# Kernel tuning notes

Measured on AMD Instinct MI355X. Metric: run time of the kernel, lower is better.

Reference implementation:

```python
import jax, jax.numpy as jnp
from jax import lax
import numpy as np

NUM_GROUPS = 16
GN_EPS = 1e-5
POOL = 4
CLAMP_MIN, CLAMP_MAX = 0.0, 1.0


def setup_inputs() -> dict:
    key = jax.random.key(0)
    ks = jax.random.split(key, 6)
    B, Cin, H, W = 128, 8, 128, 128
    Cout, K = 64, 3
    return {
        "x": jax.random.normal(ks[0], (B, Cin, H, W), dtype=jnp.float32),
        "conv_weight": jax.random.normal(ks[1], (Cout, Cin, K, K), dtype=jnp.float32) * 0.1,
        "conv_bias": jax.random.normal(ks[2], (Cout,), dtype=jnp.float32) * 0.1,
        "gn_weight": jax.random.normal(ks[3], (Cout,), dtype=jnp.float32) * 0.1 + 1.0,
        "gn_bias": jax.random.normal(ks[4], (Cout,), dtype=jnp.float32) * 0.1,
        "scale": jax.random.normal(ks[5], (Cout, 1, 1), dtype=jnp.float32) * 0.1 + 1.0,
    }


def reference(x, conv_weight, conv_bias, gn_weight, gn_bias, scale):
    # Conv2d, stride=1, padding=0 (VALID)
    y = lax.conv_general_dilated(
        x, conv_weight, window_strides=(1, 1), padding="VALID",
        dimension_numbers=("NCHW", "OIHW", "NCHW"))
    y = y + conv_bias[None, :, None, None]
    B, C, H, W = y.shape  # (128, 64, 126, 126)
    # GroupNorm: stats per (sample, group)
    yg = y.reshape(B, NUM_GROUPS, -1)
    mean = jnp.mean(yg, axis=-1, keepdims=True)
    var = jnp.mean(jnp.square(yg - mean), axis=-1, keepdims=True)
    yn = ((yg - mean) * lax.rsqrt(var + GN_EPS)).reshape(B, C, H, W)
    yn = yn * gn_weight[None, :, None, None] + gn_bias[None, :, None, None]
    # per-channel scale, shape (C,1,1)
    yn = yn * scale[None]
    # MaxPool2d(kernel=4, stride=4, no padding, floor mode)
    p = lax.reduce_window(yn, -jnp.inf, lax.max,
                          window_dimensions=(1, 1, POOL, POOL),
                          window_strides=(1, 1, POOL, POOL),
                          padding="VALID")
    return jnp.clip(p, CLAMP_MIN, CLAMP_MAX)
```

## Files before the change

kernel.cpp:

```cpp
#include <hip/hip_runtime.h>

typedef __attribute__((ext_vector_type(8))) short short8v;
typedef __attribute__((ext_vector_type(4))) float f32x4;
typedef __attribute__((ext_vector_type(4))) int i32x4;

#define BATCH 128
#define CIN 8
#define HW 128
#define COUT 64
#define OHW 126
#define NG 16
#define PH 31
#define GN_EPS 1e-5f

#define ROWS_A 8
#define STRIPS_A 16
#define INROWS_A 11
#define ACOLS 132

static __device__ __forceinline__ unsigned short f2bf(float f) {
    unsigned u = __float_as_uint(f);
    return (unsigned short)((u + 0x7fffu + ((u >> 16) & 1u)) >> 16);
}
static __device__ __forceinline__ unsigned pk2(float a, float b) {
    return (unsigned)f2bf(a) | ((unsigned)f2bf(b) << 16);
}

__global__ __launch_bounds__(256) void prep_weights(
    const float* __restrict__ w, const float* __restrict__ gnw,
    const float* __restrict__ scale, short* __restrict__ Bpack)
{
    for (int e = threadIdx.x; e < 3 * 4 * 64; e += 256) {
        int dx = e >> 8;
        int nt = (e >> 6) & 3;
        int l  = e & 63;
        int i = l & 15, g = l >> 4;
        int n = nt * 16 + i;
        float sg = copysignf(1.f, gnw[n] * scale[n]);
        #pragma unroll
        for (int j = 0; j < 8; ++j) {
            float v = (g < 3) ? w[((n * CIN + j) * 3 + g) * 3 + dx] * sg : 0.f;
            Bpack[e * 8 + j] = (short)f2bf(v);
        }
    }
}

__global__ __launch_bounds__(256, 4) void conv_fused(
    const float* __restrict__ x, const short* __restrict__ Bpack,
    const float* __restrict__ bias, const float* __restrict__ gnw,
    const float* __restrict__ scale, float* __restrict__ part,
    float* __restrict__ mzbuf)
{
    __shared__ __align__(16) short Abuf[INROWS_A][ACOLS][8];
    __shared__ float red[4][NG][2];
    const int strip = blockIdx.x, b = blockIdx.y;
    const int tid = threadIdx.x, wave = tid >> 6, lane = tid & 63;
    const int i = lane & 15, g = lane >> 4;
    const int r0 = strip * ROWS_A;

    short8v bq[3][4];
    {
        const i32x4* bp = (const i32x4*)Bpack;
        #pragma unroll
        for (int dx = 0; dx < 3; ++dx)
            #pragma unroll
            for (int nt = 0; nt < 4; ++nt) {
                i32x4 v = bp[(dx * 4 + nt) * 64 + lane];
                bq[dx][nt] = *(short8v*)&v;
            }
    }
    float sgn[4], bs2[4], bsg[4];
    #pragma unroll
    for (int nt = 0; nt < 4; ++nt) {
        int c = nt * 16 + i;
        float bc = bias[c];
        float sg = copysignf(1.f, gnw[c] * scale[c]);
        sgn[nt] = sg;
        bs2[nt] = 2.f * bc;
        bsg[nt] = sg * bc;
    }

    {
        const float* xb = x + (size_t)b * CIN * HW * HW;
        for (int e = tid; e < INROWS_A * ACOLS; e += 256) {
            int row = e / ACOLS, col = e % ACOLS;
            int ri = r0 + row;
            bool ok = (row < 10) && (ri < HW) && (col < HW);
            unsigned pk0, pk1, pk2_, pk3;
            {
                const float* base = &xb[(size_t)ri * HW + col];
                float v0 = ok ? base[0 * HW * HW] : 0.f;
                float v1 = ok ? base[1 * HW * HW] : 0.f;
                float v2 = ok ? base[2 * HW * HW] : 0.f;
                float v3 = ok ? base[3 * HW * HW] : 0.f;
                float v4 = ok ? base[4 * HW * HW] : 0.f;
                float v5 = ok ? base[5 * HW * HW] : 0.f;
                float v6 = ok ? base[6 * HW * HW] : 0.f;
                float v7 = ok ? base[7 * HW * HW] : 0.f;
                pk0  = pk2(v0, v1);
                pk1  = pk2(v2, v3);
                pk2_ = pk2(v4, v5);
                pk3  = pk2(v6, v7);
            }
            uint4 w4 = make_uint4(pk0, pk1, pk2_, pk3);
            *(uint4*)&Abuf[row][col][0] = w4;
        }
    }
    __syncthreads();

    float s1[4] = {0.f, 0.f, 0.f, 0.f}, s2[4] = {0.f, 0.f, 0.f, 0.f};
    const int myprow = wave & 1;
    const int tbase  = (wave >> 1) * 4;
    const int prow_g = strip * 2 + myprow;

    for (int tl = 0; tl < 4; ++tl) {
        const int t = tbase + tl;
        float mz[4] = {-3e38f, -3e38f, -3e38f, -3e38f};
        #pragma unroll
        for (int ri_ = 0; ri_ < 4; ++ri_) {
            const int rloc = 4 * myprow + ri_;
            if (r0 + rloc < OHW) {
                f32x4 acc[4];
                #pragma unroll
                for (int nt = 0; nt < 4; ++nt) acc[nt] = (f32x4){0.f, 0.f, 0.f, 0.f};
                #pragma unroll
                for (int dx = 0; dx < 3; ++dx) {
                    short8v a = *(const short8v*)&Abuf[rloc + g][16 * t + i + dx][0];
                    #pragma unroll
                    for (int nt = 0; nt < 4; ++nt)
                        acc[nt] = __builtin_amdgcn_mfma_f32_16x16x32_bf16(a, bq[dx][nt], acc[nt], 0, 0, 0);
                }
                const int nv = (t == 7 && g == 3) ? 2 : 4;
                #pragma unroll
                for (int nt = 0; nt < 4; ++nt) {
                    #pragma unroll
                    for (int r = 0; r < 4; ++r)
                        if (r < nv) {
                            float a = acc[nt][r];
                            s1[nt] += a;
                            s2[nt] = fmaf(a, a, s2[nt]);
                        }
                    mz[nt] = fmaxf(mz[nt],
                             fmaxf(fmaxf(acc[nt][0], acc[nt][1]),
                                   fmaxf(acc[nt][2], acc[nt][3])));
                }
            }
        }
        const int pc = 4 * t + g;
        if (prow_g < PH && pc < PH) {
            float* dst = &mzbuf[((size_t)(b * PH + prow_g) * 32 + pc) * 64 + i];
            #pragma unroll
            for (int nt = 0; nt < 4; ++nt) dst[nt * 16] = mz[nt] + bsg[nt];
        }
    }

    #pragma unroll
    for (int nt = 0; nt < 4; ++nt) {
        float t1 = s1[nt] * sgn[nt];
        s2[nt] = fmaf(bs2[nt], t1, s2[nt]);
        s1[nt] = t1;
    }
    #pragma unroll
    for (int nt = 0; nt < 4; ++nt) {
        s1[nt] += __shfl_xor(s1[nt], 1);  s1[nt] += __shfl_xor(s1[nt], 2);
        s1[nt] += __shfl_xor(s1[nt], 16); s1[nt] += __shfl_xor(s1[nt], 32);
        s2[nt] += __shfl_xor(s2[nt], 1);  s2[nt] += __shfl_xor(s2[nt], 2);
        s2[nt] += __shfl_xor(s2[nt], 16); s2[nt] += __shfl_xor(s2[nt], 32);
    }
    if (g == 0 && (i & 3) == 0) {
        #pragma unroll
        for (int nt = 0; nt < 4; ++nt) {
            red[wave][nt * 4 + (i >> 2)][0] = s1[nt];
            red[wave][nt * 4 + (i >> 2)][1] = s2[nt];
        }
    }
    __syncthreads();
    if (tid < 32) {
        int grp = tid >> 1, which = tid & 1;
        float v = red[0][grp][which] + red[1][grp][which] + red[2][grp][which] + red[3][grp][which];
        part[(((size_t)b * STRIPS_A + strip) * NG + grp) * 2 + which] = v;
    }
}

__global__ __launch_bounds__(256) void finalize_affine(
    const float* __restrict__ part, const float* __restrict__ gnw,
    const float* __restrict__ gnb, const float* __restrict__ scale,
    const float* __restrict__ bias, const float* __restrict__ mzbuf,
    float* __restrict__ out)
{
    __shared__ float sl[PH * 65];
    __shared__ float A2s[COUT], Bvs[COUT];
    const int ph = blockIdx.x, b = blockIdx.y;
    const int tid = threadIdx.x;

    if (tid < COUT) {
        const int c = tid, grp = c >> 2;
        float s1 = 0.f, s2 = 0.f;
        for (int s = 0; s < STRIPS_A; ++s) {
            const float* p = &part[(((size_t)b * STRIPS_A + s) * NG + grp) * 2];
            s1 += p[0]; s2 += p[1];
        }
        float sumb = 0.f, sumb2 = 0.f;
        #pragma unroll
        for (int ci = 0; ci < 4; ++ci) {
            float bc = bias[grp * 4 + ci];
            sumb += bc; sumb2 += bc * bc;
        }
        const float N1 = (float)(OHW * OHW);
        float S1 = s1 + N1 * sumb;
        float S2 = s2 + N1 * sumb2;
        const float invN = 1.f / (4.f * N1);
        float mean = S1 * invN;
        float var  = S2 * invN - mean * mean;
        float rstd = rsqrtf(var + GN_EPS);
        float gs = gnw[c] * scale[c];
        A2s[c] = rstd * fabsf(gs);
        Bvs[c] = (gnb[c] - mean * rstd * gnw[c]) * scale[c];
    }

    const float* src = mzbuf + (size_t)(b * PH + ph) * 32 * 64;
    for (int e = tid; e < PH * 64; e += 256) {
        int pc = e >> 6, c = e & 63;
        sl[pc * 65 + c] = src[pc * 64 + c];
    }
    __syncthreads();

    const int c = tid >> 2, q = tid & 3;
    const float A2 = A2s[c];
    const float B0 = Bvs[c];
    float* ob = out + (size_t)(b * COUT + c) * (PH * PH) + ph * PH;
    #pragma unroll
    for (int k = 0; k < 8; ++k) {
        int pw = q * 8 + k;
        if (pw < PH) {
            float v = fmaf(A2, sl[pw * 65 + c], B0);
            ob[pw] = fminf(fmaxf(v, 0.f), 1.f);
        }
    }
}

extern "C" void kernel_launch(void* const* d_in, const int* in_sizes, int n_in,
                              void* d_out, int out_size, void* d_ws, size_t ws_size,
                              hipStream_t stream)
{
    const float* x   = (const float*)d_in[0];
    const float* w   = (const float*)d_in[1];
    const float* cbv = (const float*)d_in[2];
    const float* gnw = (const float*)d_in[3];
    const float* gnb = (const float*)d_in[4];
    const float* sc  = (const float*)d_in[5];
    float* out = (float*)d_out;

    float* mzbuf = (float*)d_ws;
    float* part  = mzbuf + (size_t)BATCH * PH * 32 * 64;
    short* Bpack = (short*)(part + 65536);

    prep_weights<<<dim3(1), 256, 0, stream>>>(w, gnw, sc, Bpack);
    conv_fused<<<dim3(STRIPS_A, BATCH), 256, 0, stream>>>(x, Bpack, cbv, gnw, sc, part, mzbuf);
    finalize_affine<<<dim3(PH, BATCH), 256, 0, stream>>>(part, gnw, gnb, sc, cbv, mzbuf, out);
}
```

Before: 66.58 us.

## Switch conv MFMA from 16x16x32 to 32x32x16 bf16 tiles

Recasts the implicit-GEMM convolution to use 32x32x16 bf16 MFMA instructions instead of 16x16x32. The K dimension (dy x Cin) is split into two chunks across lane halves, and the output channels are split into two 32-wide tiles. The weight packing, the accumulator layout, the max-pool reduction over the 16 accumulator registers and the GroupNorm statistics shuffles are all remapped to match. The aim is fewer MFMA issues and A-operand LDS loads per output, at the cost of larger accumulators that raise register pressure. The layout remapping also adds correctness risk.

```diff
diff --git a/kernel.cpp b/kernel.cpp
--- a/kernel.cpp
+++ b/kernel.cpp
@@ -1,7 +1,7 @@
 #include <hip/hip_runtime.h>
 
 typedef __attribute__((ext_vector_type(8))) short short8v;
-typedef __attribute__((ext_vector_type(4))) float f32x4;
+typedef __attribute__((ext_vector_type(16))) float f32x16;
 typedef __attribute__((ext_vector_type(4))) int i32x4;
 
 #define BATCH 128
@@ -30,16 +30,16 @@
     const float* __restrict__ w, const float* __restrict__ gnw,
     const float* __restrict__ scale, short* __restrict__ Bpack)
 {
-    for (int e = threadIdx.x; e < 3 * 4 * 64; e += 256) {
-        int dx = e >> 8;
-        int nt = (e >> 6) & 3;
+    for (int e = threadIdx.x; e < 12 * 64; e += 256) {
+        int f  = e >> 6;
         int l  = e & 63;
-        int i = l & 15, g = l >> 4;
-        int n = nt * 16 + i;
+        int dx = f >> 2, kk = (f >> 1) & 1, nt = f & 1;
+        int n  = nt * 32 + (l & 31);
+        int dy = kk * 2 + (l >> 5);
         float sg = copysignf(1.f, gnw[n] * scale[n]);
         #pragma unroll
         for (int j = 0; j < 8; ++j) {
-            float v = (g < 3) ? w[((n * CIN + j) * 3 + g) * 3 + dx] * sg : 0.f;
+            float v = (dy < 3) ? w[((n * CIN + j) * 3 + dy) * 3 + dx] * sg : 0.f;
             Bpack[e * 8 + j] = (short)f2bf(v);
         }
     }
@@ -55,24 +55,26 @@
     __shared__ float red[4][NG][2];
     const int strip = blockIdx.x, b = blockIdx.y;
     const int tid = threadIdx.x, wave = tid >> 6, lane = tid & 63;
-    const int i = lane & 15, g = lane >> 4;
+    const int h = lane >> 5, m31 = lane & 31;
     const int r0 = strip * ROWS_A;
 
-    short8v bq[3][4];
+    short8v bq[3][2][2];
     {
         const i32x4* bp = (const i32x4*)Bpack;
         #pragma unroll
         for (int dx = 0; dx < 3; ++dx)
             #pragma unroll
-            for (int nt = 0; nt < 4; ++nt) {
-                i32x4 v = bp[(dx * 4 + nt) * 64 + lane];
-                bq[dx][nt] = *(short8v*)&v;
-            }
-    }
-    float sgn[4], bs2[4], bsg[4];
+            for (int kk = 0; kk < 2; ++kk)
+                #pragma unroll
+                for (int nt = 0; nt < 2; ++nt) {
+                    i32x4 v = bp[(dx * 4 + kk * 2 + nt) * 64 + lane];
+                    bq[dx][kk][nt] = *(short8v*)&v;
+                }
+    }
+    float sgn[2], bs2[2], bsg[2];
     #pragma unroll
-    for (int nt = 0; nt < 4; ++nt) {
-        int c = nt * 16 + i;
+    for (int nt = 0; nt < 2; ++nt) {
+        int c = nt * 32 + m31;
         float bc = bias[c];
         float sg = copysignf(1.f, gnw[c] * scale[c]);
         sgn[nt] = sg;
@@ -108,71 +110,77 @@
     }
     __syncthreads();
 
-    float s1[4] = {0.f, 0.f, 0.f, 0.f}, s2[4] = {0.f, 0.f, 0.f, 0.f};
+    float s1[2] = {0.f, 0.f}, s2[2] = {0.f, 0.f};
     const int myprow = wave & 1;
-    const int tbase  = (wave >> 1) * 4;
+    const int thalf  = wave >> 1;
     const int prow_g = strip * 2 + myprow;
 
-    for (int tl = 0; tl < 4; ++tl) {
-        const int t = tbase + tl;
-        float mz[4] = {-3e38f, -3e38f, -3e38f, -3e38f};
+    for (int tt = 0; tt < 2; ++tt) {
+        const int t32 = thalf * 2 + tt;
+        const int colbase = 32 * t32 + m31;
+        float mzw[2][4];
+        #pragma unroll
+        for (int nt = 0; nt < 2; ++nt)
+            #pragma unroll
+            for (int q = 0; q < 4; ++q) mzw[nt][q] = -3e38f;
+
         #pragma unroll
         for (int ri_ = 0; ri_ < 4; ++ri_) {
             const int rloc = 4 * myprow + ri_;
             if (r0 + rloc < OHW) {
-                f32x4 acc[4];
+                f32x16 acc0 = {0.f,0.f,0.f,0.f,0.f,0.f,0.f,0.f,0.f,0.f,0.f,0.f,0.f,0.f,0.f,0.f};
+                f32x16 acc1 = {0.f,0.f,0.f,0.f,0.f,0.f,0.f,0.f,0.f,0.f,0.f,0.f,0.f,0.f,0.f,0.f};
                 #pragma unroll
-                for (int nt = 0; nt < 4; ++nt) acc[nt] = (f32x4){0.f, 0.f, 0.f, 0.f};
+                for (int kk = 0; kk < 2; ++kk) {
+                    const int arow = rloc + kk * 2 + h;
+                    #pragma unroll
+                    for (int dx = 0; dx < 3; ++dx) {
+                        short8v a = *(const short8v*)&Abuf[arow][colbase + dx][0];
+                        acc0 = __builtin_amdgcn_mfma_f32_32x32x16_bf16(a, bq[dx][kk][0], acc0, 0, 0, 0);
+                        acc1 = __builtin_amdgcn_mfma_f32_32x32x16_bf16(a, bq[dx][kk][1], acc1, 0, 0, 0);
+                    }
+                }
+                const bool hi = (t32 == 3) && (h == 1);
                 #pragma unroll
-                for (int dx = 0; dx < 3; ++dx) {
-                    short8v a = *(const short8v*)&Abuf[rloc + g][16 * t + i + dx][0];
-                    #pragma unroll
-                    for (int nt = 0; nt < 4; ++nt)
-                        acc[nt] = __builtin_amdgcn_mfma_f32_16x16x32_bf16(a, bq[dx][nt], acc[nt], 0, 0, 0);
-                }
-                const int nv = (t == 7 && g == 3) ? 2 : 4;
-                #pragma unroll
-                for (int nt = 0; nt < 4; ++nt) {
-                    #pragma unroll
-                    for (int r = 0; r < 4; ++r)
-                        if (r < nv) {
-                            float a = acc[nt][r];
-                            s1[nt] += a;
-                            s2[nt] = fmaf(a, a, s2[nt]);
-                        }
-                    mz[nt] = fmaxf(mz[nt],
-                             fmaxf(fmaxf(acc[nt][0], acc[nt][1]),
-                                   fmaxf(acc[nt][2], acc[nt][3])));
+                for (int r = 0; r < 16; ++r) {
+                    float a0 = acc0[r], a1 = acc1[r];
+                    if (!(hi && r >= 14)) {
+                        s1[0] += a0; s2[0] = fmaf(a0, a0, s2[0]);
+                        s1[1] += a1; s2[1] = fmaf(a1, a1, s2[1]);
+                    }
+                    mzw[0][r >> 2] = fmaxf(mzw[0][r >> 2], a0);
+                    mzw[1][r >> 2] = fmaxf(mzw[1][r >> 2], a1);
                 }
             }
         }
-        const int pc = 4 * t + g;
-        if (prow_g < PH && pc < PH) {
-            float* dst = &mzbuf[((size_t)(b * PH + prow_g) * 32 + pc) * 64 + i];
+        if (prow_g < PH) {
             #pragma unroll
-            for (int nt = 0; nt < 4; ++nt) dst[nt * 16] = mz[nt] + bsg[nt];
+            for (int q = 0; q < 4; ++q) {
+                const int pc = 8 * t32 + 2 * q + h;
+                if (pc < PH) {
+                    float* dst = &mzbuf[((size_t)(b * PH + prow_g) * 32 + pc) * 64 + m31];
+                    dst[0]  = mzw[0][q] + bsg[0];
+                    dst[32] = mzw[1][q] + bsg[1];
+                }
+            }
         }
     }
 
     #pragma unroll
-    for (int nt = 0; nt < 4; ++nt) {
+    for (int nt = 0; nt < 2; ++nt) {
         float t1 = s1[nt] * sgn[nt];
         s2[nt] = fmaf(bs2[nt], t1, s2[nt]);
         s1[nt] = t1;
-    }
-    #pragma unroll
-    for (int nt = 0; nt < 4; ++nt) {
+        s1[nt] += __shfl_xor(s1[nt], 32);
         s1[nt] += __shfl_xor(s1[nt], 1);  s1[nt] += __shfl_xor(s1[nt], 2);
-        s1[nt] += __shfl_xor(s1[nt], 16); s1[nt] += __shfl_xor(s1[nt], 32);
+        s2[nt] += __shfl_xor(s2[nt], 32);
         s2[nt] += __shfl_xor(s2[nt], 1);  s2[nt] += __shfl_xor(s2[nt], 2);
-        s2[nt] += __shfl_xor(s2[nt], 16); s2[nt] += __shfl_xor(s2[nt], 32);
-    }
-    if (g == 0 && (i & 3) == 0) {
-        #pragma unroll
-        for (int nt = 0; nt < 4; ++nt) {
-            red[wave][nt * 4 + (i >> 2)][0] = s1[nt];
-            red[wave][nt * 4 + (i >> 2)][1] = s2[nt];
-        }
+    }
+    if (lane < 32 && (lane & 3) == 0) {
+        red[wave][(m31 >> 2)][0]     = s1[0];
+        red[wave][(m31 >> 2)][1]     = s2[0];
+        red[wave][8 + (m31 >> 2)][0] = s1[1];
+        red[wave][8 + (m31 >> 2)][1] = s2[1];
     }
     __syncthreads();
     if (tid < 32) {
```

New measurement: 64.52 us (median of 2 runs). 1.03x faster.
